# Performance work log

Measured on AMD Instinct MI355X. Metric: run time of the kernel, lower is better.

The kernel has to match this reference:

```python
import jax, jax.numpy as jnp
import numpy as np

# dims: D=embed_dim (= number of experts), H=heads, P=image patches, Q=query embeddings, B=batch
D, H, N, P, B, Q = 256, 8, 256, 1024, 1, 64
HD = D // H
EPS = 1e-5


def _ln(x, g, b):
    m = x.mean(-1, keepdims=True)
    v = x.var(-1, keepdims=True)
    return (x - m) / jnp.sqrt(v + EPS) * g + b


def _mha(q_x, kv_x, Wqkv, bqkv, Wo, bo):
    # standard torch nn.MultiheadAttention (batch_first, eval mode)
    Wq, Wk, Wv = jnp.split(Wqkv, 3, axis=0)
    bq, bk, bv = jnp.split(bqkv, 3, axis=0)
    q = q_x @ Wq.T + bq
    k = kv_x @ Wk.T + bk
    v = kv_x @ Wv.T + bv
    Bq, S, _ = q.shape
    Sk = k.shape[1]
    qh = q.reshape(Bq, S, H, HD)
    kh = k.reshape(Bq, Sk, H, HD)
    vh = v.reshape(Bq, Sk, H, HD)
    att = jax.nn.softmax(jnp.einsum('bqhd,bkhd->bhqk', qh, kh) / np.sqrt(HD).astype(np.float32), axis=-1)
    ctx = jnp.einsum('bhqk,bkhd->bqhd', att, vh).reshape(Bq, S, D)
    return ctx @ Wo.T + bo


def setup_inputs() -> dict:
    key = jax.random.key(0)
    ks = jax.random.split(key, 12)
    s = 0.02  # weight init scale
    return {
        'image_patches': jax.random.normal(ks[0], (B, P, D), jnp.float32),
        'expert_tokens': jax.random.normal(ks[1], (B, N, D), jnp.float32),
        'query_embeddings': jax.random.normal(ks[2], (B, Q, D), jnp.float32),
        'Wqkv_experts': jax.random.normal(ks[3], (N, 3 * D, D), jnp.float32) * s,
        'bqkv_experts': jnp.zeros((N, 3 * D), jnp.float32),
        'Wo_experts': jax.random.normal(ks[4], (N, D, D), jnp.float32) * s,
        'bo_experts': jnp.zeros((N, D), jnp.float32),
        'Wqkv_q': jax.random.normal(ks[5], (3 * D, D), jnp.float32) * s,
        'bqkv_q': jnp.zeros((3 * D,), jnp.float32),
        'Wo_q': jax.random.normal(ks[6], (D, D), jnp.float32) * s,
        'bo_q': jnp.zeros((D,), jnp.float32),
        'Wqkv_s': jax.random.normal(ks[7], (3 * D, D), jnp.float32) * s,
        'bqkv_s': jnp.zeros((3 * D,), jnp.float32),
        'Wo_s': jax.random.normal(ks[8], (D, D), jnp.float32) * s,
        'bo_s': jnp.zeros((D,), jnp.float32),
        'W1': jax.random.normal(ks[9], (4 * D, D), jnp.float32) * s,
        'b1': jnp.zeros((4 * D,), jnp.float32),
        'W2': jax.random.normal(ks[10], (D, 4 * D), jnp.float32) * s,
        'b2': jnp.zeros((D,), jnp.float32),
        'ln1_g': jnp.ones((D,), jnp.float32), 'ln1_b': jnp.zeros((D,), jnp.float32),
        'ln2_g': jnp.ones((D,), jnp.float32), 'ln2_b': jnp.zeros((D,), jnp.float32),
        'ln3_g': jnp.ones((D,), jnp.float32), 'ln3_b': jnp.zeros((D,), jnp.float32),
    }


def reference(image_patches, expert_tokens, query_embeddings,
              Wqkv_experts, bqkv_experts, Wo_experts, bo_experts,
              Wqkv_q, bqkv_q, Wo_q, bo_q,
              Wqkv_s, bqkv_s, Wo_s, bo_s,
              W1, b1, W2, b2,
              ln1_g, ln1_b, ln2_g, ln2_b, ln3_g, ln3_b):
    # --- per-expert cross attention (the embed_dim separate MHA calls, fused/batched) ---
    Wq, Wk, Wv = jnp.split(Wqkv_experts, 3, axis=1)   # each [N, D, D]
    bq, bk, bv = jnp.split(bqkv_experts, 3, axis=1)   # each [N, D]
    q = jnp.einsum('bnd,ned->bne', expert_tokens, Wq) + bq                       # [B,N,D]
    K = jnp.einsum('bpd,ned->bnpe', image_patches, Wk) + bk[None, :, None, :]    # [B,N,P,D]
    V = jnp.einsum('bpd,ned->bnpe', image_patches, Wv) + bv[None, :, None, :]    # [B,N,P,D]
    qh = q.reshape(B, N, H, HD)
    Kh = K.reshape(B, N, P, H, HD)
    Vh = V.reshape(B, N, P, H, HD)
    att = jax.nn.softmax(jnp.einsum('bnhd,bnphd->bnhp', qh, Kh) / np.sqrt(HD).astype(np.float32), axis=-1)
    image_attention_weights = att.mean(axis=2)        # [B,N,P] head-averaged, torch default
    ctx = jnp.einsum('bnhp,bnphd->bnhd', att, Vh).reshape(B, N, D)
    attended_image = jnp.einsum('bnd,ned->bne', ctx, Wo_experts) + bo_experts    # [B,N,D]
    attended_image = _ln(attended_image + expert_tokens, ln1_g, ln1_b)
    # --- query cross attention ---
    attended_query = _mha(attended_image, query_embeddings, Wqkv_q, bqkv_q, Wo_q, bo_q)
    attended_query = _ln(attended_query + attended_image, ln2_g, ln2_b)
    # --- FFN (no residual in original) ---
    expert_refined = jax.nn.relu(attended_query @ W1.T + b1) @ W2.T + b2
    # --- expert self attention + residual + norm ---
    sa = _mha(expert_refined, expert_refined, Wqkv_s, bqkv_s, Wo_s, bo_s)
    expert_features = _ln(sa + expert_refined, ln3_g, ln3_b)
    return expert_features, image_attention_weights
```

## Files before the change

kernel.cpp:

```cpp
#include <hip/hip_runtime.h>

#define DD 256
#define NH 8
#define NP 1024
#define NQ 64
#define SCALE 0.17677669529663687f

typedef float f32x4v __attribute__((ext_vector_type(4)));
typedef __bf16 bfv8 __attribute__((ext_vector_type(8)));

union BF8 { bfv8 v; unsigned short u16[8]; uint4 q; };

__device__ __forceinline__ float wred_sum(float p) {
  #pragma unroll
  for (int m = 32; m; m >>= 1) p += __shfl_xor(p, m);
  return p;
}
__device__ __forceinline__ float wred_max(float p) {
  #pragma unroll
  for (int m = 32; m; m >>= 1) p = fmaxf(p, __shfl_xor(p, m));
  return p;
}
__device__ __forceinline__ float red8(float p) {
  p += __shfl_xor(p, 1);
  p += __shfl_xor(p, 2);
  p += __shfl_xor(p, 4);
  return p;
}
__device__ __forceinline__ float dot4(float4 a, float4 b) {
  return a.x*b.x + a.y*b.y + a.z*b.z + a.w*b.w;
}
__device__ __forceinline__ float4 ldnt4(const float* p) {
  f32x4v v = __builtin_nontemporal_load((const f32x4v*)p);
  return make_float4(v.x, v.y, v.z, v.w);
}
__device__ __forceinline__ unsigned short f2b(float f) {
  unsigned int u = __float_as_uint(f);
  u += 0x7fffu + ((u >> 16) & 1u);
  return (unsigned short)(u >> 16);
}
__device__ __forceinline__ BF8 cvt8(float4 a, float4 b) {
  BF8 r;
  r.u16[0]=f2b(a.x); r.u16[1]=f2b(a.y); r.u16[2]=f2b(a.z); r.u16[3]=f2b(a.w);
  r.u16[4]=f2b(b.x); r.u16[5]=f2b(b.y); r.u16[6]=f2b(b.z); r.u16[7]=f2b(b.w);
  return r;
}
__device__ __forceinline__ f32x4v mfma16(BF8 a, BF8 b, f32x4v c) {
  return __builtin_amdgcn_mfma_f32_16x16x32_bf16(a.v, b.v, c, 0, 0, 0);
}

__device__ __forceinline__ void preload8(const float* x, int lane, float4* xf) {
  const int o = (lane & 7) * 4;
  #pragma unroll
  for (int cc = 0; cc < 8; ++cc) xf[cc] = *(const float4*)&x[cc*32 + o];
}
template<bool NT>
__device__ __forceinline__ void pass16(const float* __restrict__ W, int ldk,
                                       int r0, int lane, const float4* xf,
                                       float* outA, float* outB) {
  const float* baseA = W + (size_t)(r0 + (lane >> 3))*ldk + (lane & 7)*4;
  const float* baseB = baseA + (size_t)8*ldk;
  float4 wa[8], wb[8];
  #pragma unroll
  for (int cc = 0; cc < 8; ++cc) wa[cc] = NT ? ldnt4(&baseA[cc*32]) : *(const float4*)&baseA[cc*32];
  #pragma unroll
  for (int cc = 0; cc < 8; ++cc) wb[cc] = NT ? ldnt4(&baseB[cc*32]) : *(const float4*)&baseB[cc*32];
  float a = 0.f, b = 0.f;
  #pragma unroll
  for (int cc = 0; cc < 8; ++cc) { a += dot4(wa[cc], xf[cc]); b += dot4(wb[cc], xf[cc]); }
  *outA = red8(a); *outB = red8(b);
}

__device__ __forceinline__ void layernorm_store(const float* buf, float* outp,
                                                const float* g, const float* b,
                                                float* red, int tid, int wid, int lane)
{
  __syncthreads();
  if (wid == 0) {
    float s = buf[lane] + buf[lane+64] + buf[lane+128] + buf[lane+192];
    s = wred_sum(s);
    if (!lane) red[0] = s * (1.f/256.f);
  }
  __syncthreads();
  float mn = red[0];
  if (wid == 0) {
    float d0 = buf[lane]-mn, d1 = buf[lane+64]-mn, d2 = buf[lane+128]-mn, d3 = buf[lane+192]-mn;
    float s = d0*d0 + d1*d1 + d2*d2 + d3*d3;
    s = wred_sum(s);
    if (!lane) red[1] = rsqrtf(s * (1.f/256.f) + 1e-5f);
  }
  __syncthreads();
  if (tid < 256) outp[tid] = (buf[tid] - mn) * red[1] * g[tid] + b[tid];
}

__global__ __launch_bounds__(256)
void k_pre(const float* __restrict__ patches, uint4* __restrict__ pTB,
           uint4* __restrict__ patchesB,
           const float* __restrict__ qe, const float* __restrict__ Wqkv_q,
           const float* __restrict__ bqkv_q, float* __restrict__ kvq)
{
  const int b = blockIdx.x, tid = threadIdx.x;
  if (b < 128) {
    const int T = b*4 + (tid >> 6), l = tid & 63;
    const int kt = T >> 6, nt = T & 63;
    const int row = nt*16 + (l & 15), col = kt*32 + (l >> 4)*8;
    float4 a = *(const float4*)&patches[(size_t)row*DD + col];
    float4 c = *(const float4*)&patches[(size_t)row*DD + col + 4];
    pTB[(size_t)T*64 + l] = cvt8(a, c).q;
  } else if (b < 256) {
    const int T = (b - 128)*4 + (tid >> 6), l = tid & 63;
    const int kt = T >> 4, nt = T & 15;
    const int col = nt*16 + (l & 15), p0 = kt*32 + (l >> 4)*8;
    float v[8];
    #pragma unroll
    for (int j = 0; j < 8; ++j) v[j] = patches[(size_t)(p0 + j)*DD + col];
    BF8 r;
    #pragma unroll
    for (int j = 0; j < 8; ++j) r.u16[j] = f2b(v[j]);
    patchesB[(size_t)T*64 + l] = r.q;
  } else {
    __shared__ float x[DD], kvrow[512];
    const int j = b - 256, w = tid >> 6, lane = tid & 63;
    if (tid < DD) x[tid] = qe[j*DD + tid];
    __syncthreads();
    float4 xf[8]; preload8(x, lane, xf);
    #pragma unroll
    for (int g = 0; g < 8; ++g) {
      int r0 = w*128 + g*16;
      float a, bb;
      pass16<false>(Wqkv_q + (size_t)DD*DD, DD, r0, lane, xf, &a, &bb);
      int rA = r0 + (lane >> 3);
      if ((lane & 7) == 0) {
        kvrow[rA]   = a  + bqkv_q[DD + rA];
        kvrow[rA+8] = bb + bqkv_q[DD + rA + 8];
      }
    }
    __syncthreads();
    kvq[(size_t)j*512 + tid]       = kvrow[tid];
    kvq[(size_t)j*512 + 256 + tid] = kvrow[256 + tid];
  }
}

__global__ __launch_bounds__(512)
void k_front(const float* __restrict__ et_g,
             const float* __restrict__ Wqkv_e, const float* __restrict__ bqkv_e,
             const uint4* __restrict__ pTB, const uint4* __restrict__ patchesB,
             float* __restrict__ ctx_ws, float* __restrict__ iaw)
{
  const int n = blockIdx.x, tid = threadIdx.x, w = tid >> 6, lane = tid & 63;
  __shared__ float xL[DD], qL[DD];
  __shared__ float attS[NH][NP];
  __shared__ __align__(16) char uAbuf[32768];
  __shared__ float uS[NH][DD];
  float (*tS)[260] = (float (*)[260])uAbuf;
  uint4 (*attB)[128] = (uint4 (*)[128])uAbuf;

  const float* Wn = Wqkv_e + (size_t)n*(3*DD*DD);
  const float* bn = bqkv_e + (size_t)n*(3*DD);

  if (tid < DD) xL[tid] = et_g[(size_t)n*DD + tid];
  __syncthreads();

  {
    float4 xf[8]; preload8(xL, lane, xf);
    #pragma unroll
    for (int g = 0; g < 2; ++g) {
      float a, bq;
      pass16<true>(Wn, DD, w*32 + g*16, lane, xf, &a, &bq);
      int rA = w*32 + g*16 + (lane >> 3);
      if ((lane & 7) == 0) { qL[rA] = a + bn[rA]; qL[rA+8] = bq + bn[rA+8]; }
    }
  }
  {
    const float* Wk = Wn + (size_t)DD*DD + (size_t)w*32*DD;
    float4 acc = make_float4(0.f, 0.f, 0.f, 0.f);
    #pragma unroll 8
    for (int r = 0; r < 32; ++r) {
      float qs = qL[w*32 + r];
      float4 wv = ldnt4(&Wk[(size_t)r*DD + 4*lane]);
      acc.x += qs*wv.x; acc.y += qs*wv.y; acc.z += qs*wv.z; acc.w += qs*wv.w;
    }
    *(float4*)&tS[w][4*lane] = acc;
  }
  __syncthreads();

  BF8 afr[8];
  {
    const int rr = lane & 15, ko = (lane >> 4)*8;
    #pragma unroll
    for (int kt = 0; kt < 8; ++kt) {
      float4 a = *(const float4*)&tS[rr][kt*32 + ko];
      float4 c = *(const float4*)&tS[rr][kt*32 + ko + 4];
      afr[kt] = cvt8(a, c);
    }
  }
  {
    #pragma unroll
    for (int t8 = 0; t8 < 8; ++t8) {
      const int nt = w*8 + t8;
      f32x4v acc = {0.f, 0.f, 0.f, 0.f};
      #pragma unroll
      for (int kt = 0; kt < 8; ++kt) {
        BF8 bb; bb.q = pTB[(size_t)(kt*64 + nt)*64 + lane];
        acc = mfma16(afr[kt], bb, acc);
      }
      if (lane < 32) {
        const int r0 = (lane >> 4)*4, cc = nt*16 + (lane & 15);
        #pragma unroll
        for (int i = 0; i < 4; ++i) attS[r0 + i][cc] = acc[i];
      }
    }
  }
  __syncthreads();

  {
    const int h = w;
    float v[16];
    #pragma unroll
    for (int k = 0; k < 16; ++k) v[k] = attS[h][k*64 + lane] * SCALE;
    float mx = v[0];
    #pragma unroll
    for (int k = 1; k < 16; ++k) mx = fmaxf(mx, v[k]);
    mx = wred_max(mx);
    float sum = 0.f;
    #pragma unroll
    for (int k = 0; k < 16; ++k) { v[k] = __expf(v[k] - mx); sum += v[k]; }
    sum = wred_sum(sum);
    float rinv = 1.f / sum;
    #pragma unroll
    for (int k = 0; k < 16; ++k) attS[h][k*64 + lane] = v[k] * rinv;
  }
  __syncthreads();

  #pragma unroll
  for (int rep = 0; rep < 2; ++rep) {
    int p = rep*512 + tid;
    float s = 0.f;
    #pragma unroll
    for (int h = 0; h < NH; ++h) s += attS[h][p];
    iaw[(size_t)n*NP + p] = s * 0.125f;
  }
  #pragma unroll
  for (int rep = 0; rep < 2; ++rep) {
    int C = rep*512 + tid;
    int row = C >> 7, c = C & 127;
    float4 a = *(const float4*)&attS[row][c*8];
    float4 b = *(const float4*)&attS[row][c*8 + 4];
    int swz = (c & ~7) | ((c ^ row) & 7);
    attB[row][swz] = cvt8(a, b).q;
  }
  __syncthreads();

  {
    const int nt0 = 2*w, nt1 = 2*w + 1;
    f32x4v acc0 = {0.f,0.f,0.f,0.f}, acc1 = {0.f,0.f,0.f,0.f};
    const int rr = lane & 15, cq = lane >> 4;
    #pragma unroll 8
    for (int kt = 0; kt < 32; ++kt) {
      int cc = kt*4 + cq;
      int swz = (cc & ~7) | ((cc ^ rr) & 7);
      BF8 a;  a.q  = attB[rr][swz];
      BF8 b0; b0.q = patchesB[(size_t)(kt*16 + nt0)*64 + lane];
      BF8 b1; b1.q = patchesB[(size_t)(kt*16 + nt1)*64 + lane];
      acc0 = mfma16(a, b0, acc0);
      acc1 = mfma16(a, b1, acc1);
    }
    if (lane < 32) {
      const int r0 = (lane >> 4)*4;
      #pragma unroll
      for (int i = 0; i < 4; ++i) {
        uS[r0+i][nt0*16 + (lane & 15)] = acc0[i];
        uS[r0+i][nt1*16 + (lane & 15)] = acc1[i];
      }
    }
  }
  __syncthreads();

  {
    float4 xf[8]; preload8(&uS[w][0], lane, xf);
    #pragma unroll
    for (int g = 0; g < 2; ++g) {
      float a, bq;
      pass16<true>(Wn + (size_t)2*DD*DD, DD, w*32 + g*16, lane, xf, &a, &bq);
      int rA = w*32 + g*16 + (lane >> 3);
      if ((lane & 7) == 0) {
        ctx_ws[(size_t)n*DD + rA]     = a  + bn[2*DD + rA];
        ctx_ws[(size_t)n*DD + rA + 8] = bq + bn[2*DD + rA + 8];
      }
    }
  }
}

__global__ __launch_bounds__(1024)
void k_mid(const float* __restrict__ ctx_ws, const float* __restrict__ et_g,
           const float* __restrict__ Wo_e, const float* __restrict__ bo_e,
           const float* __restrict__ kvq,
           const float* __restrict__ Wqkv_q, const float* __restrict__ bqkv_q,
           const float* __restrict__ Wo_q, const float* __restrict__ bo_q,
           const float* __restrict__ W1, const float* __restrict__ b1,
           const float* __restrict__ W2, const float* __restrict__ b2,
           const float* __restrict__ Wqkv_s, const float* __restrict__ bqkv_s,
           const float* __restrict__ ln1g, const float* __restrict__ ln1b,
           const float* __restrict__ ln2g, const float* __restrict__ ln2b,
           float* __restrict__ er_g, float* __restrict__ qkvs_g)
{
  const int n = blockIdx.x, tid = threadIdx.x, w = tid >> 6, lane = tid & 63;
  __shared__ float xL[DD], qL[DD], ctxL[DD], resS[DD], attq[NH][NQ], red2[2];
  __shared__ float hb[1024], qrow[768];

  if (tid < DD) { ctxL[tid] = ctx_ws[(size_t)n*DD + tid]; xL[tid] = et_g[(size_t)n*DD + tid]; }
  __syncthreads();

  {
    float4 xf[8]; preload8(ctxL, lane, xf);
    const float* Won = Wo_e + (size_t)n*DD*DD;
    float a, b;
    pass16<true>(Won, DD, w*16, lane, xf, &a, &b);
    int rA = w*16 + (lane >> 3);
    if ((lane & 7) == 0) {
      resS[rA]   = a + bo_e[(size_t)n*DD + rA]     + xL[rA];
      resS[rA+8] = b + bo_e[(size_t)n*DD + rA + 8] + xL[rA+8];
    }
  }
  layernorm_store(resS, xL, ln1g, ln1b, red2, tid, w, lane);
  __syncthreads();

  {
    float4 xf[8]; preload8(xL, lane, xf);
    float a, b;
    pass16<false>(Wqkv_q, DD, w*16, lane, xf, &a, &b);
    int rA = w*16 + (lane >> 3);
    if ((lane & 7) == 0) { qL[rA] = a + bqkv_q[rA]; qL[rA+8] = b + bqkv_q[rA+8]; }
  }
  __syncthreads();
  if (w < 8) {
    const int h = w, j = lane;
    float4 q4[8];
    #pragma unroll
    for (int m = 0; m < 8; ++m) q4[m] = *(const float4*)&qL[h*32 + 4*m];
    const float* kj = kvq + (size_t)j*512 + h*32;
    float s = 0.f;
    #pragma unroll
    for (int m = 0; m < 8; ++m) s += dot4(*(const float4*)&kj[4*m], q4[m]);
    s *= SCALE;
    float mx = wred_max(s);
    float p = __expf(s - mx);
    float sum = wred_sum(p);
    attq[h][j] = p / sum;
  }
  __syncthreads();
  if (tid < DD) {
    const int rr = tid, h = rr >> 5;
    float acc = 0.f;
    #pragma unroll 4
    for (int j4 = 0; j4 < 16; ++j4) {
      float4 a4 = *(const float4*)&attq[h][j4*4];
      acc += a4.x * kvq[(size_t)(j4*4+0)*512 + DD + rr]
           + a4.y * kvq[(size_t)(j4*4+1)*512 + DD + rr]
           + a4.z * kvq[(size_t)(j4*4+2)*512 + DD + rr]
           + a4.w * kvq[(size_t)(j4*4+3)*512 + DD + rr];
    }
    ctxL[rr] = acc;
  }
  __syncthreads();
  {
    float4 xf[8]; preload8(ctxL, lane, xf);
    float a, b;
    pass16<false>(Wo_q, DD, w*16, lane, xf, &a, &b);
    int rA = w*16 + (lane >> 3);
    if ((lane & 7) == 0) { resS[rA] = a + bo_q[rA] + xL[rA]; resS[rA+8] = b + bo_q[rA+8] + xL[rA+8]; }
  }
  layernorm_store(resS, xL, ln2g, ln2b, red2, tid, w, lane);
  __syncthreads();

  {
    float4 xf[8]; preload8(xL, lane, xf);
    #pragma unroll
    for (int g = 0; g < 4; ++g) {
      int r0 = w*64 + g*16;
      float a, b;
      pass16<false>(W1, DD, r0, lane, xf, &a, &b);
      int rA = r0 + (lane >> 3);
      if ((lane & 7) == 0) { hb[rA] = fmaxf(a + b1[rA], 0.f); hb[rA+8] = fmaxf(b + b1[rA+8], 0.f); }
    }
  }
  __syncthreads();
  {
    float accA = 0.f, accB = 0.f;
    #pragma unroll
    for (int kc = 0; kc < 4; ++kc) {
      float4 xh[8]; preload8(hb + kc*256, lane, xh);
      float a, b;
      pass16<false>(W2 + kc*256, 1024, w*16, lane, xh, &a, &b);
      accA += a; accB += b;
    }
    int rA = w*16 + (lane >> 3);
    if ((lane & 7) == 0) { qL[rA] = accA + b2[rA]; qL[rA+8] = accB + b2[rA+8]; }
  }
  __syncthreads();
  {
    float4 xf[8]; preload8(qL, lane, xf);
    #pragma unroll
    for (int g = 0; g < 3; ++g) {
      int r0 = w*48 + g*16;
      float a, b;
      pass16<false>(Wqkv_s, DD, r0, lane, xf, &a, &b);
      int rA = r0 + (lane >> 3);
      if ((lane & 7) == 0) { qrow[rA] = a + bqkv_s[rA]; qrow[rA+8] = b + bqkv_s[rA+8]; }
    }
  }
  __syncthreads();
  if (tid < 768) qkvs_g[(size_t)n*768 + tid] = qrow[tid];
  if (tid < DD)  er_g[(size_t)n*DD + tid]   = qL[tid];
}

__global__ __launch_bounds__(1024)
void k_sa(const float* __restrict__ er, const float* __restrict__ qkvs,
          const float* __restrict__ Wo_s, const float* __restrict__ bo_s,
          const float* __restrict__ ln3g, const float* __restrict__ ln3b,
          float* __restrict__ ef)
{
  const int i = blockIdx.x, tid = threadIdx.x, w = tid >> 6, lane = tid & 63;
  __shared__ float x[DD], attl[NH][256], ctxp[4][DD], resS[DD], red2[2];
  if (tid < DD) x[tid] = er[(size_t)i*DD + tid];
  {
    const int h = w & 7, kh = w >> 3;
    float4 q4[8];
    #pragma unroll
    for (int m = 0; m < 8; ++m) q4[m] = *(const float4*)&qkvs[(size_t)i*768 + h*32 + 4*m];
    #pragma unroll
    for (int rep = 0; rep < 2; ++rep) {
      int j = kh*128 + rep*64 + lane;
      const float* kj = qkvs + (size_t)j*768 + DD + h*32;
      float4 k4[8];
      #pragma unroll
      for (int m = 0; m < 8; ++m) k4[m] = *(const float4*)&kj[4*m];
      float s = 0.f;
      #pragma unroll
      for (int m = 0; m < 8; ++m) s += dot4(k4[m], q4[m]);
      attl[h][j] = s * SCALE;
    }
  }
  __syncthreads();
  if (w < 8) {
    const int h = w;
    float v0 = attl[h][lane], v1 = attl[h][lane+64], v2 = attl[h][lane+128], v3 = attl[h][lane+192];
    float mx = wred_max(fmaxf(fmaxf(v0,v1), fmaxf(v2,v3)));
    float e0 = __expf(v0-mx), e1 = __expf(v1-mx), e2 = __expf(v2-mx), e3 = __expf(v3-mx);
    float sum = wred_sum(e0+e1+e2+e3);
    float r = 1.f/sum;
    attl[h][lane] = e0*r; attl[h][lane+64] = e1*r; attl[h][lane+128] = e2*r; attl[h][lane+192] = e3*r;
  }
  __syncthreads();
  {
    const int rr = tid & 255, qtr = tid >> 8, h = rr >> 5;
    float acc = 0.f;
    #pragma unroll 4
    for (int j4 = qtr*16; j4 < qtr*16 + 16; ++j4) {
      float4 a4 = *(const float4*)&attl[h][j4*4];
      acc += a4.x * qkvs[(size_t)(j4*4+0)*768 + 512 + rr]
           + a4.y * qkvs[(size_t)(j4*4+1)*768 + 512 + rr]
           + a4.z * qkvs[(size_t)(j4*4+2)*768 + 512 + rr]
           + a4.w * qkvs[(size_t)(j4*4+3)*768 + 512 + rr];
    }
    ctxp[qtr][rr] = acc;
  }
  __syncthreads();
  {
    float4 xf[8];
    const int o = (lane & 7)*4;
    #pragma unroll
    for (int cc = 0; cc < 8; ++cc) {
      float4 a = *(const float4*)&ctxp[0][cc*32 + o];
      float4 b = *(const float4*)&ctxp[1][cc*32 + o];
      float4 c = *(const float4*)&ctxp[2][cc*32 + o];
      float4 d = *(const float4*)&ctxp[3][cc*32 + o];
      xf[cc] = make_float4(a.x+b.x+c.x+d.x, a.y+b.y+c.y+d.y,
                           a.z+b.z+c.z+d.z, a.w+b.w+c.w+d.w);
    }
    float a, b;
    pass16<false>(Wo_s, DD, w*16, lane, xf, &a, &b);
    int rA = w*16 + (lane >> 3);
    if ((lane & 7) == 0) { resS[rA] = a + bo_s[rA] + x[rA]; resS[rA+8] = b + bo_s[rA+8] + x[rA+8]; }
  }
  layernorm_store(resS, ef + (size_t)i*DD, ln3g, ln3b, red2, tid, w, lane);
}

extern "C" void kernel_launch(void* const* d_in, const int* in_sizes, int n_in,
                              void* d_out, int out_size, void* d_ws, size_t ws_size,
                              hipStream_t stream) {
  const float* patches = (const float*)d_in[0];
  const float* et      = (const float*)d_in[1];
  const float* qe      = (const float*)d_in[2];
  const float* Wqkv_e  = (const float*)d_in[3];
  const float* bqkv_e  = (const float*)d_in[4];
  const float* Wo_e    = (const float*)d_in[5];
  const float* bo_e    = (const float*)d_in[6];
  const float* Wqkv_q  = (const float*)d_in[7];
  const float* bqkv_q  = (const float*)d_in[8];
  const float* Wo_q    = (const float*)d_in[9];
  const float* bo_q    = (const float*)d_in[10];
  const float* Wqkv_s  = (const float*)d_in[11];
  const float* bqkv_s  = (const float*)d_in[12];
  const float* Wo_s    = (const float*)d_in[13];
  const float* bo_s    = (const float*)d_in[14];
  const float* W1      = (const float*)d_in[15];
  const float* b1      = (const float*)d_in[16];
  const float* W2      = (const float*)d_in[17];
  const float* b2      = (const float*)d_in[18];
  const float* ln1g = (const float*)d_in[19]; const float* ln1b = (const float*)d_in[20];
  const float* ln2g = (const float*)d_in[21]; const float* ln2b = (const float*)d_in[22];
  const float* ln3g = (const float*)d_in[23]; const float* ln3b = (const float*)d_in[24];

  float* ef  = (float*)d_out;
  float* iaw = (float*)d_out + 65536;

  float* ws       = (float*)d_ws;
  uint4* pTB      = (uint4*)ws;
  uint4* patchesB = (uint4*)(ws + 131072);
  float* kvq      = ws + 262144;
  float* ctx_ws   = ws + 294912;
  float* er       = ws + 360448;
  float* qkvs     = ws + 425984;

  k_pre<<<320, 256, 0, stream>>>(patches, pTB, patchesB, qe, Wqkv_q, bqkv_q, kvq);
  k_front<<<256, 512, 0, stream>>>(et, Wqkv_e, bqkv_e, pTB, patchesB, ctx_ws, iaw);
  k_mid<<<256, 1024, 0, stream>>>(ctx_ws, et, Wo_e, bo_e,
                                  kvq, Wqkv_q, bqkv_q, Wo_q, bo_q,
                                  W1, b1, W2, b2, Wqkv_s, bqkv_s,
                                  ln1g, ln1b, ln2g, ln2b, er, qkvs);
  k_sa<<<256, 1024, 0, stream>>>(er, qkvs, Wo_s, bo_s, ln3g, ln3b, ef);
}
```

Measured before the change: 155.3 us.

## Convert shared mid-stage weights to bf16 and move expert Wo+LN1 into k_front

k_pre now converts the shared weights Wqkv_q, Wo_q, W1, W2 and Wqkv_s to bf16 in workspace. k_mid's GEMVs read these through a new bf16 dot path, halving weight bytes that all 256 blocks re-read from cache. The per-expert Wo projection plus LayerNorm1 moves from k_mid into k_front, so ctx no longer round-trips through global memory. Nontemporal loads on expert weights are dropped. The trade-offs are a larger k_pre grid with extra conversion work, reduced weight precision, and heavier k_front blocks.

Result: faster. 136.6 us (median of 2 runs) (-12.0%).

```diff
diff --git a/kernel.cpp b/kernel.cpp
--- a/kernel.cpp
+++ b/kernel.cpp
@@ -30,10 +30,6 @@
 __device__ __forceinline__ float dot4(float4 a, float4 b) {
   return a.x*b.x + a.y*b.y + a.z*b.z + a.w*b.w;
 }
-__device__ __forceinline__ float4 ldnt4(const float* p) {
-  f32x4v v = __builtin_nontemporal_load((const f32x4v*)p);
-  return make_float4(v.x, v.y, v.z, v.w);
-}
 __device__ __forceinline__ unsigned short f2b(float f) {
   unsigned int u = __float_as_uint(f);
   u += 0x7fffu + ((u >> 16) & 1u);
@@ -48,13 +44,20 @@
 __device__ __forceinline__ f32x4v mfma16(BF8 a, BF8 b, f32x4v c) {
   return __builtin_amdgcn_mfma_f32_16x16x32_bf16(a.v, b.v, c, 0, 0, 0);
 }
+__device__ __forceinline__ float2 b2f2(unsigned int u) {
+  return make_float2(__uint_as_float(u << 16), __uint_as_float(u & 0xffff0000u));
+}
+__device__ __forceinline__ float dotb8(uint4 w, float4 x0, float4 x1) {
+  float2 p0 = b2f2(w.x), p1 = b2f2(w.y), p2 = b2f2(w.z), p3 = b2f2(w.w);
+  return p0.x*x0.x + p0.y*x0.y + p1.x*x0.z + p1.y*x0.w
+       + p2.x*x1.x + p2.y*x1.y + p3.x*x1.z + p3.y*x1.w;
+}
 
 __device__ __forceinline__ void preload8(const float* x, int lane, float4* xf) {
   const int o = (lane & 7) * 4;
   #pragma unroll
   for (int cc = 0; cc < 8; ++cc) xf[cc] = *(const float4*)&x[cc*32 + o];
 }
-template<bool NT>
 __device__ __forceinline__ void pass16(const float* __restrict__ W, int ldk,
                                        int r0, int lane, const float4* xf,
                                        float* outA, float* outB) {
@@ -62,12 +65,38 @@
   const float* baseB = baseA + (size_t)8*ldk;
   float4 wa[8], wb[8];
   #pragma unroll
-  for (int cc = 0; cc < 8; ++cc) wa[cc] = NT ? ldnt4(&baseA[cc*32]) : *(const float4*)&baseA[cc*32];
-  #pragma unroll
-  for (int cc = 0; cc < 8; ++cc) wb[cc] = NT ? ldnt4(&baseB[cc*32]) : *(const float4*)&baseB[cc*32];
+  for (int cc = 0; cc < 8; ++cc) wa[cc] = *(const float4*)&baseA[cc*32];
+  #pragma unroll
+  for (int cc = 0; cc < 8; ++cc) wb[cc] = *(const float4*)&baseB[cc*32];
   float a = 0.f, b = 0.f;
   #pragma unroll
   for (int cc = 0; cc < 8; ++cc) { a += dot4(wa[cc], xf[cc]); b += dot4(wb[cc], xf[cc]); }
+  *outA = red8(a); *outB = red8(b);
+}
+__device__ __forceinline__ void preload8b(const float* x, int lane, float4* xf) {
+  const int o = (lane & 7) * 8;
+  #pragma unroll
+  for (int cc = 0; cc < 4; ++cc) {
+    xf[2*cc]   = *(const float4*)&x[cc*64 + o];
+    xf[2*cc+1] = *(const float4*)&x[cc*64 + o + 4];
+  }
+}
+__device__ __forceinline__ void pass16b(const unsigned short* __restrict__ W, int ldk,
+                                        int r0, int lane, const float4* xf,
+                                        float* outA, float* outB) {
+  const unsigned short* baseA = W + (size_t)(r0 + (lane >> 3))*ldk + (lane & 7)*8;
+  const unsigned short* baseB = baseA + (size_t)8*ldk;
+  uint4 wa[4], wb[4];
+  #pragma unroll
+  for (int cc = 0; cc < 4; ++cc) wa[cc] = *(const uint4*)&baseA[cc*64];
+  #pragma unroll
+  for (int cc = 0; cc < 4; ++cc) wb[cc] = *(const uint4*)&baseB[cc*64];
+  float a = 0.f, b = 0.f;
+  #pragma unroll
+  for (int cc = 0; cc < 4; ++cc) {
+    a += dotb8(wa[cc], xf[2*cc], xf[2*cc+1]);
+    b += dotb8(wb[cc], xf[2*cc], xf[2*cc+1]);
+  }
   *outA = red8(a); *outB = red8(b);
 }
 
@@ -97,7 +126,10 @@
 void k_pre(const float* __restrict__ patches, uint4* __restrict__ pTB,
            uint4* __restrict__ patchesB,
            const float* __restrict__ qe, const float* __restrict__ Wqkv_q,
-           const float* __restrict__ bqkv_q, float* __restrict__ kvq)
+           const float* __restrict__ bqkv_q, float* __restrict__ kvq,
+           const float* __restrict__ Wo_q, const float* __restrict__ W1,
+           const float* __restrict__ W2, const float* __restrict__ Wqkv_s,
+           unsigned short* __restrict__ wsB)
 {
   const int b = blockIdx.x, tid = threadIdx.x;
   if (b < 128) {
@@ -118,7 +150,7 @@
     #pragma unroll
     for (int j = 0; j < 8; ++j) r.u16[j] = f2b(v[j]);
     patchesB[(size_t)T*64 + l] = r.q;
-  } else {
+  } else if (b < 320) {
     __shared__ float x[DD], kvrow[512];
     const int j = b - 256, w = tid >> 6, lane = tid & 63;
     if (tid < DD) x[tid] = qe[j*DD + tid];
@@ -128,7 +160,7 @@
     for (int g = 0; g < 8; ++g) {
       int r0 = w*128 + g*16;
       float a, bb;
-      pass16<false>(Wqkv_q + (size_t)DD*DD, DD, r0, lane, xf, &a, &bb);
+      pass16(Wqkv_q + (size_t)DD*DD, DD, r0, lane, xf, &a, &bb);
       int rA = r0 + (lane >> 3);
       if ((lane & 7) == 0) {
         kvrow[rA]   = a  + bqkv_q[DD + rA];
@@ -138,17 +170,31 @@
     __syncthreads();
     kvq[(size_t)j*512 + tid]       = kvrow[tid];
     kvq[(size_t)j*512 + 256 + tid] = kvrow[256 + tid];
+  } else {
+    const int gid = (b - 320)*256 + tid;
+    const float* src;
+    size_t dof;
+    if      (gid < 8192)  { src = Wqkv_q + (size_t)gid*8;           dof = (size_t)gid*8; }
+    else if (gid < 16384) { src = Wo_q   + (size_t)(gid-8192)*8;    dof = 65536  + (size_t)(gid-8192)*8; }
+    else if (gid < 49152) { src = W1     + (size_t)(gid-16384)*8;   dof = 131072 + (size_t)(gid-16384)*8; }
+    else if (gid < 81920) { src = W2     + (size_t)(gid-49152)*8;   dof = 393216 + (size_t)(gid-49152)*8; }
+    else                  { src = Wqkv_s + (size_t)(gid-81920)*8;   dof = 655360 + (size_t)(gid-81920)*8; }
+    float4 a = *(const float4*)&src[0];
+    float4 c = *(const float4*)&src[4];
+    *(uint4*)&wsB[dof] = cvt8(a, c).q;
   }
 }
 
 __global__ __launch_bounds__(512)
 void k_front(const float* __restrict__ et_g,
              const float* __restrict__ Wqkv_e, const float* __restrict__ bqkv_e,
+             const float* __restrict__ Wo_e, const float* __restrict__ bo_e,
              const uint4* __restrict__ pTB, const uint4* __restrict__ patchesB,
-             float* __restrict__ ctx_ws, float* __restrict__ iaw)
+             const float* __restrict__ ln1g, const float* __restrict__ ln1b,
+             float* __restrict__ aln_g, float* __restrict__ iaw)
 {
   const int n = blockIdx.x, tid = threadIdx.x, w = tid >> 6, lane = tid & 63;
-  __shared__ float xL[DD], qL[DD];
+  __shared__ float xL[DD], qL[DD], ctxL[DD], resS[DD], red2[2];
   __shared__ float attS[NH][NP];
   __shared__ __align__(16) char uAbuf[32768];
   __shared__ float uS[NH][DD];
@@ -166,7 +212,7 @@
     #pragma unroll
     for (int g = 0; g < 2; ++g) {
       float a, bq;
-      pass16<true>(Wn, DD, w*32 + g*16, lane, xf, &a, &bq);
+      pass16(Wn, DD, w*32 + g*16, lane, xf, &a, &bq);
       int rA = w*32 + g*16 + (lane >> 3);
       if ((lane & 7) == 0) { qL[rA] = a + bn[rA]; qL[rA+8] = bq + bn[rA+8]; }
     }
@@ -177,7 +223,7 @@
     #pragma unroll 8
     for (int r = 0; r < 32; ++r) {
       float qs = qL[w*32 + r];
-      float4 wv = ldnt4(&Wk[(size_t)r*DD + 4*lane]);
+      float4 wv = *(const float4*)&Wk[(size_t)r*DD + 4*lane];
       acc.x += qs*wv.x; acc.y += qs*wv.y; acc.z += qs*wv.z; acc.w += qs*wv.w;
     }
     *(float4*)&tS[w][4*lane] = acc;
@@ -281,54 +327,55 @@
     #pragma unroll
     for (int g = 0; g < 2; ++g) {
       float a, bq;
-      pass16<true>(Wn + (size_t)2*DD*DD, DD, w*32 + g*16, lane, xf, &a, &bq);
+      pass16(Wn + (size_t)2*DD*DD, DD, w*32 + g*16, lane, xf, &a, &bq);
+      int rA = w*32 + g*16 + (lane >> 3);
+      if ((lane & 7) == 0) { ctxL[rA] = a + bn[2*DD + rA]; ctxL[rA+8] = bq + bn[2*DD + rA + 8]; }
+    }
+  }
+  __syncthreads();
+
+  {
+    float4 xf[8]; preload8(ctxL, lane, xf);
+    const float* Won = Wo_e + (size_t)n*DD*DD;
+    #pragma unroll
+    for (int g = 0; g < 2; ++g) {
+      float a, bq;
+      pass16(Won, DD, w*32 + g*16, lane, xf, &a, &bq);
       int rA = w*32 + g*16 + (lane >> 3);
       if ((lane & 7) == 0) {
-        ctx_ws[(size_t)n*DD + rA]     = a  + bn[2*DD + rA];
-        ctx_ws[(size_t)n*DD + rA + 8] = bq + bn[2*DD + rA + 8];
+        resS[rA]   = a  + bo_e[(size_t)n*DD + rA]     + xL[rA];
+        resS[rA+8] = bq + bo_e[(size_t)n*DD + rA + 8] + xL[rA+8];
       }
     }
   }
+  layernorm_store(resS, aln_g + (size_t)n*DD, ln1g, ln1b, red2, tid, w, lane);
 }
 
 __global__ __launch_bounds__(1024)
-void k_mid(const float* __restrict__ ctx_ws, const float* __restrict__ et_g,
-           const float* __restrict__ Wo_e, const float* __restrict__ bo_e,
-           const float* __restrict__ kvq,
-           const float* __restrict__ Wqkv_q, const float* __restrict__ bqkv_q,
-           const float* __restrict__ Wo_q, const float* __restrict__ bo_q,
-           const float* __restrict__ W1, const float* __restrict__ b1,
-           const float* __restrict__ W2, const float* __restrict__ b2,
-           const float* __restrict__ Wqkv_s, const float* __restrict__ bqkv_s,
-           const float* __restrict__ ln1g, const float* __restrict__ ln1b,
+void k_mid(const float* __restrict__ aln, const float* __restrict__ kvq,
+           const unsigned short* __restrict__ wsB,
+           const float* __restrict__ bqkv_q, const float* __restrict__ bo_q,
+           const float* __restrict__ b1, const float* __restrict__ b2,
+           const float* __restrict__ bqkv_s,
            const float* __restrict__ ln2g, const float* __restrict__ ln2b,
            float* __restrict__ er_g, float* __restrict__ qkvs_g)
 {
   const int n = blockIdx.x, tid = threadIdx.x, w = tid >> 6, lane = tid & 63;
   __shared__ float xL[DD], qL[DD], ctxL[DD], resS[DD], attq[NH][NQ], red2[2];
   __shared__ float hb[1024], qrow[768];
-
-  if (tid < DD) { ctxL[tid] = ctx_ws[(size_t)n*DD + tid]; xL[tid] = et_g[(size_t)n*DD + tid]; }
-  __syncthreads();
-
-  {
-    float4 xf[8]; preload8(ctxL, lane, xf);
-    const float* Won = Wo_e + (size_t)n*DD*DD;
+  const unsigned short* WqB  = wsB;
+  const unsigned short* WoqB = wsB + 65536;
+  const unsigned short* W1B  = wsB + 131072;
+  const unsigned short* W2B  = wsB + 393216;
+  const unsigned short* WsB  = wsB + 655360;
+
+  if (tid < DD) xL[tid] = aln[(size_t)n*DD + tid];
+  __syncthreads();
+
+  {
+    float4 xf[8]; preload8b(xL, lane, xf);
     float a, b;
-    pass16<true>(Won, DD, w*16, lane, xf, &a, &b);
-    int rA = w*16 + (lane >> 3);
-    if ((lane & 7) == 0) {
-      resS[rA]   = a + bo_e[(size_t)n*DD + rA]     + xL[rA];
-      resS[rA+8] = b + bo_e[(size_t)n*DD + rA + 8] + xL[rA+8];
-    }
-  }
-  layernorm_store(resS, xL, ln1g, ln1b, red2, tid, w, lane);
-  __syncthreads();
-
-  {
-    float4 xf[8]; preload8(xL, lane, xf);
-    float a, b;
-    pass16<false>(Wqkv_q, DD, w*16, lane, xf, &a, &b);
+    pass16b(WqB, DD, w*16, lane, xf, &a, &b);
     int rA = w*16 + (lane >> 3);
     if ((lane & 7) == 0) { qL[rA] = a + bqkv_q[rA]; qL[rA+8] = b + bqkv_q[rA+8]; }
   }
@@ -364,9 +411,9 @@
   }
   __syncthreads();
   {
-    float4 xf[8]; preload8(ctxL, lane, xf);
+    float4 xf[8]; preload8b(ctxL, lane, xf);
     float a, b;
-    pass16<false>(Wo_q, DD, w*16, lane, xf, &a, &b);
+    pass16b(WoqB, DD, w*16, lane, xf, &a, &b);
     int rA = w*16 + (lane >> 3);
     if ((lane & 7) == 0) { resS[rA] = a + bo_q[rA] + xL[rA]; resS[rA+8] = b + bo_q[rA+8] + xL[rA+8]; }
   }
@@ -374,12 +421,12 @@
   __syncthreads();
 
   {
-    float4 xf[8]; preload8(xL, lane, xf);
+    float4 xf[8]; preload8b(xL, lane, xf);
     #pragma unroll
     for (int g = 0; g < 4; ++g) {
       int r0 = w*64 + g*16;
       float a, b;
-      pass16<false>(W1, DD, r0, lane, xf, &a, &b);
+      pass16b(W1B, DD, r0, lane, xf, &a, &b);
       int rA = r0 + (lane >> 3);
       if ((lane & 7) == 0) { hb[rA] = fmaxf(a + b1[rA], 0.f); hb[rA+8] = fmaxf(b + b1[rA+8], 0.f); }
     }
@@ -389,9 +436,9 @@
     float accA = 0.f, accB = 0.f;
     #pragma unroll
     for (int kc = 0; kc < 4; ++kc) {
-      float4 xh[8]; preload8(hb + kc*256, lane, xh);
+      float4 xh[8]; preload8b(hb + kc*256, lane, xh);
       float a, b;
-      pass16<false>(W2 + kc*256, 1024, w*16, lane, xh, &a, &b);
+      pass16b(W2B + kc*256, 1024, w*16, lane, xh, &a, &b);
       accA += a; accB += b;
     }
     int rA = w*16 + (lane >> 3);
@@ -399,12 +446,12 @@
   }
   __syncthreads();
   {
-    float4 xf[8]; preload8(qL, lane, xf);
+    float4 xf[8]; preload8b(qL, lane, xf);
     #pragma unroll
     for (int g = 0; g < 3; ++g) {
       int r0 = w*48 + g*16;
       float a, b;
-      pass16<false>(Wqkv_s, DD, r0, lane, xf, &a, &b);
+      pass16b(WsB, DD, r0, lane, xf, &a, &b);
       int rA = r0 + (lane >> 3);
       if ((lane & 7) == 0) { qrow[rA] = a + bqkv_s[rA]; qrow[rA+8] = b + bqkv_s[rA+8]; }
     }
@@ -479,7 +526,7 @@
                            a.z+b.z+c.z+d.z, a.w+b.w+c.w+d.w);
     }
     float a, b;
-    pass16<false>(Wo_s, DD, w*16, lane, xf, &a, &b);
+    pass16(Wo_s, DD, w*16, lane, xf, &a, &b);
     int rA = w*16 + (lane >> 3);
     if ((lane & 7) == 0) { resS[rA] = a + bo_s[rA] + x[rA]; resS[rA+8] = b + bo_s[rA+8] + x[rA+8]; }
   }
@@ -515,19 +562,20 @@
   float* ef  = (float*)d_out;
   float* iaw = (float*)d_out + 65536;
 
-  float* ws       = (float*)d_ws;
-  uint4* pTB      = (uint4*)ws;
-  uint4* patchesB = (uint4*)(ws + 131072);
-  float* kvq      = ws + 262144;
-  float* ctx_ws   = ws + 294912;
-  float* er       = ws + 360448;
-  float* qkvs     = ws + 425984;
-
-  k_pre<<<320, 256, 0, stream>>>(patches, pTB, patchesB, qe, Wqkv_q, bqkv_q, kvq);
-  k_front<<<256, 512, 0, stream>>>(et, Wqkv_e, bqkv_e, pTB, patchesB, ctx_ws, iaw);
-  k_mid<<<256, 1024, 0, stream>>>(ctx_ws, et, Wo_e, bo_e,
-                                  kvq, Wqkv_q, bqkv_q, Wo_q, bo_q,
-                                  W1, b1, W2, b2, Wqkv_s, bqkv_s,
-                                  ln1g, ln1b, ln2g, ln2b, er, qkvs);
+  float* ws           = (float*)d_ws;
+  uint4* pTB          = (uint4*)ws;
+  uint4* patchesB     = (uint4*)(ws + 131072);
+  float* kvq          = ws + 262144;
+  float* aln          = ws + 294912;
+  float* er           = ws + 360448;
+  float* qkvs         = ws + 425984;
+  unsigned short* wsB = (unsigned short*)(ws + 622592);
+
+  k_pre<<<736, 256, 0, stream>>>(patches, pTB, patchesB, qe, Wqkv_q, bqkv_q, kvq,
+                                 Wo_q, W1, W2, Wqkv_s, wsB);
+  k_front<<<256, 512, 0, stream>>>(et, Wqkv_e, bqkv_e, Wo_e, bo_e,
+                                   pTB, patchesB, ln1g, ln1b, aln, iaw);
+  k_mid<<<256, 1024, 0, stream>>>(aln, kvq, wsB, bqkv_q, bo_q, b1, b2, bqkv_s,
+                                  ln2g, ln2b, er, qkvs);
   k_sa<<<256, 1024, 0, stream>>>(er, qkvs, Wo_s, bo_s, ln3g, ln3b, ef);
 }
```
